# Kernel tuning notes

Hardware: AMD Instinct MI355X
Metric: run time of the kernel (lower is better)

The kernel has to match this reference:

```python
import jax, jax.numpy as jnp
import numpy as np
from jax import lax


def _sobel3d_kernels():
    # Standard separable 3D Sobel: derivative d=[-1,0,1] along one axis,
    # smoothing s=[1,2,1] along the other two. Axes order (D, H, W).
    d = np.array([-1.0, 0.0, 1.0], dtype=np.float32)
    s = np.array([1.0, 2.0, 1.0], dtype=np.float32)
    kx = np.einsum('i,j,k->ijk', d, s, s)  # derivative along D
    ky = np.einsum('i,j,k->ijk', s, d, s)  # derivative along H
    kz = np.einsum('i,j,k->ijk', s, s, d)  # derivative along W
    # Stack as [Cout=3, Cin=1, 3, 3, 3] -> one conv computes x,y,z grads at once.
    return jnp.asarray(np.stack([kx, ky, kz])[:, None])


_DN = ('NCDHW', 'OIDHW', 'NCDHW')


def _conv3(x, k):
    # x: [N, 1, D, H, W], k: [3, 1, 3, 3, 3] -> [N, 3, D-2, H-2, W-2]
    # torch F.conv3d and lax conv are both cross-correlation; VALID padding.
    return lax.conv_general_dilated(x, k, (1, 1, 1), 'VALID', dimension_numbers=_DN)


def _g2(inp, k):
    # inp: [B, D, H, W, C] (channels last, as the torch module permutes)
    b, dd, hh, ww, c = inp.shape
    x = jnp.transpose(inp, (0, 4, 1, 2, 3)).reshape(b * c, 1, dd, hh, ww)
    g1 = _conv3(x, k)                                  # [B*C, 3, D-2, H-2, W-2]
    mag = jnp.sqrt(jnp.sum(g1 * g1, axis=1, keepdims=True))  # first-order magnitude
    g2 = _conv3(mag, k)                                # [B*C, 3, D-4, H-4, W-4]
    gx, gy, gz = g2[:, 0], g2[:, 1], g2[:, 2]
    # Faithful to source: sqrt(x^2 + y^2) + z^2 (note: z is squared, not inside sqrt)
    out = jnp.sqrt(gx * gx + gy * gy) + gz * gz        # [B*C, D-4, H-4, W-4]
    return out.reshape(b, c, *out.shape[1:])


def setup_inputs() -> dict:
    key = jax.random.key(0)
    k1, k2 = jax.random.split(key)
    pred = jax.random.normal(k1, (2, 64, 64, 64, 32), dtype=jnp.float32)
    hr = jax.random.normal(k2, (2, 64, 64, 64, 32), dtype=jnp.float32)
    return {'pred': pred, 'hr': hr}


def reference(pred, hr):
    k = _sobel3d_kernels()
    return jnp.mean(jnp.abs(_g2(pred, k) - _g2(hr, k)))
```

## Files before the change

kernel.cpp:

```cpp
#include <hip/hip_runtime.h>
#include <hip/hip_fp16.h>


constexpr int BDIM = 256;
constexpr size_t IN_B = 8388608;
constexpr int IN_D = 131072;
constexpr int IN_H = 2048;
constexpr int M = 62;
constexpr int F = 60;
constexpr int C = 32;
constexpr int MROW = M * C;
constexpr size_t MAGSZ = (size_t)M * M * MROW;
constexpr size_t PLANE = (size_t)M * MROW;

__device__ __forceinline__ float2 ld2(const float* p) {
    return *reinterpret_cast<const float2*>(p);
}
__device__ __forceinline__ float2 ldh2(const __half* p) {
    return __half22float2(*reinterpret_cast<const __half2*>(p));
}

struct P1W { float2 A[4], B[4], C[4]; };

__device__ __forceinline__ void p1_plane(const float* __restrict__ col, size_t zoff,
                                         const int jr[6], P1W& W)
{
    float2 SX[6], DX[6];
#pragma unroll
    for (int j = 0; j < 6; ++j) {
        const float* p = col + zoff + jr[j];
        float2 a = ld2(p), b = ld2(p + C), c = ld2(p + 2 * C);
        SX[j] = make_float2(a.x + 2.f * b.x + c.x, a.y + 2.f * b.y + c.y);
        DX[j] = make_float2(c.x - a.x, c.y - a.y);
    }
#pragma unroll
    for (int k = 0; k < 4; ++k) {
        W.A[k] = make_float2(SX[k].x + 2.f * SX[k+1].x + SX[k+2].x,
                             SX[k].y + 2.f * SX[k+1].y + SX[k+2].y);
        W.B[k] = make_float2(SX[k+2].x - SX[k].x, SX[k+2].y - SX[k].y);
        W.C[k] = make_float2(DX[k].x + 2.f * DX[k+1].x + DX[k+2].x,
                             DX[k].y + 2.f * DX[k+1].y + DX[k+2].y);
    }
}

__device__ __forceinline__ void p1_emit(const P1W& W0, const P1W& W1, const P1W& W2,
                                        __half* __restrict__ mag, size_t cb,
                                        int z, int y0, int kmax, bool xok)
{
    if (!xok) return;
#pragma unroll
    for (int k = 0; k < 4; ++k) {
        if (k < kmax) {
            float gxx = W2.A[k].x - W0.A[k].x;
            float gxy = W2.A[k].y - W0.A[k].y;
            float gyx = W0.B[k].x + 2.f * W1.B[k].x + W2.B[k].x;
            float gyy = W0.B[k].y + 2.f * W1.B[k].y + W2.B[k].y;
            float gzx = W0.C[k].x + 2.f * W1.C[k].x + W2.C[k].x;
            float gzy = W0.C[k].y + 2.f * W1.C[k].y + W2.C[k].y;
            float mx = sqrtf(gxx * gxx + gyx * gyx + gzx * gzx);
            float my = sqrtf(gxy * gxy + gyy * gyy + gzy * gzy);
            *reinterpret_cast<__half2*>(mag + ((size_t)z * M + (y0 + k)) * MROW + cb)
                = __floats2half2_rn(mx, my);
        }
    }
}

__global__ __launch_bounds__(BDIM) void sobel_mag_stream(
    const float* __restrict__ pred, const float* __restrict__ hr,
    __half* __restrict__ magP, __half* __restrict__ magH, int b)
{
    const int xt = blockIdx.x & 3, yt = blockIdx.x >> 2;
    const int zc = blockIdx.y;
    const float* __restrict__ in  = blockIdx.z ? hr   : pred;
    __half*      __restrict__ mag = blockIdx.z ? magH : magP;

    const int y0 = yt * 4;
    const int z0 = zc * 8;
    const int zn = min(8, M - z0);
    const int kmax = min(4, M - y0);
    const int xraw = xt * 16 + (threadIdx.x >> 4);
    const bool xok = xraw < M;
    const int x = min(xraw, M - 1);
    const int c2 = (threadIdx.x & 15) << 1;

    int jr[6];
#pragma unroll
    for (int j = 0; j < 6; ++j) jr[j] = min(y0 + j, 63) * IN_H;

    const float* col = in + (size_t)b * IN_B + (size_t)x * C + c2;
    const size_t cb = (size_t)x * C + c2;

    P1W W0, W1, W2;
    p1_plane(col, (size_t)(z0 + 0) * IN_D, jr, W0);
    p1_plane(col, (size_t)(z0 + 1) * IN_D, jr, W1);
    int z = 0;
    while (true) {
        p1_plane(col, (size_t)(z0 + z + 2) * IN_D, jr, W2);
        p1_emit(W0, W1, W2, mag, cb, z0 + z, y0, kmax, xok);
        if (++z >= zn) break;
        p1_plane(col, (size_t)(z0 + z + 2) * IN_D, jr, W0);
        p1_emit(W1, W2, W0, mag, cb, z0 + z, y0, kmax, xok);
        if (++z >= zn) break;
        p1_plane(col, (size_t)(z0 + z + 2) * IN_D, jr, W1);
        p1_emit(W2, W0, W1, mag, cb, z0 + z, y0, kmax, xok);
        if (++z >= zn) break;
    }
}

struct P2W { float2 A[2], B[2], C[2]; };

__device__ __forceinline__ void p2_plane(const __half* __restrict__ col, size_t zoff, P2W& W)
{
    float2 SX[4], DX[4];
#pragma unroll
    for (int j = 0; j < 4; ++j) {
        const __half* p = col + zoff + (size_t)j * MROW;
        float2 a = ldh2(p), b = ldh2(p + C), c = ldh2(p + 2 * C);
        SX[j] = make_float2(a.x + 2.f * b.x + c.x, a.y + 2.f * b.y + c.y);
        DX[j] = make_float2(c.x - a.x, c.y - a.y);
    }
#pragma unroll
    for (int k = 0; k < 2; ++k) {
        W.A[k] = make_float2(SX[k].x + 2.f * SX[k+1].x + SX[k+2].x,
                             SX[k].y + 2.f * SX[k+1].y + SX[k+2].y);
        W.B[k] = make_float2(SX[k+2].x - SX[k].x, SX[k+2].y - SX[k].y);
        W.C[k] = make_float2(DX[k].x + 2.f * DX[k+1].x + DX[k+2].x,
                             DX[k].y + 2.f * DX[k+1].y + DX[k+2].y);
    }
}

__device__ __forceinline__ void p2_emit(const P2W& P0, const P2W& P1, const P2W& P2,
                                        const P2W& H0, const P2W& H1, const P2W& H2,
                                        float& acc)
{
#pragma unroll
    for (int k = 0; k < 2; ++k) {
        float gxPx = P2.A[k].x - P0.A[k].x;
        float gxPy = P2.A[k].y - P0.A[k].y;
        float gyPx = P0.B[k].x + 2.f * P1.B[k].x + P2.B[k].x;
        float gyPy = P0.B[k].y + 2.f * P1.B[k].y + P2.B[k].y;
        float gzPx = P0.C[k].x + 2.f * P1.C[k].x + P2.C[k].x;
        float gzPy = P0.C[k].y + 2.f * P1.C[k].y + P2.C[k].y;
        float gxHx = H2.A[k].x - H0.A[k].x;
        float gxHy = H2.A[k].y - H0.A[k].y;
        float gyHx = H0.B[k].x + 2.f * H1.B[k].x + H2.B[k].x;
        float gyHy = H0.B[k].y + 2.f * H1.B[k].y + H2.B[k].y;
        float gzHx = H0.C[k].x + 2.f * H1.C[k].x + H2.C[k].x;
        float gzHy = H0.C[k].y + 2.f * H1.C[k].y + H2.C[k].y;
        float oPx = sqrtf(gxPx * gxPx + gyPx * gyPx) + gzPx * gzPx;
        float oPy = sqrtf(gxPy * gxPy + gyPy * gyPy) + gzPy * gzPy;
        float oHx = sqrtf(gxHx * gxHx + gyHx * gyHx) + gzHx * gzHx;
        float oHy = sqrtf(gxHy * gxHy + gyHy * gyHy) + gzHy * gzHy;
        acc += fabsf(oPx - oHx) + fabsf(oPy - oHy);
    }
}

__global__ __launch_bounds__(BDIM) void sobel2_stream(
    const __half* __restrict__ magP, const __half* __restrict__ magH,
    float* __restrict__ partial, int b)
{
    const int xt = blockIdx.x & 3, yt = blockIdx.x >> 2;
    const int zc = blockIdx.y;
    const int y0 = yt * 2;
    const int z0 = zc * 10;
    const int xraw = xt * 16 + (threadIdx.x >> 4);
    const bool xok = xraw < F;
    const int x = min(xraw, F - 1);
    const int c2 = (threadIdx.x & 15) << 1;

    const size_t colo = (size_t)y0 * MROW + (size_t)x * C + c2;
    const __half* colP = magP + colo;
    const __half* colH = magH + colo;

    P2W P0, P1, P2, H0, H1, H2;
    p2_plane(colP, (size_t)(z0 + 0) * PLANE, P0);
    p2_plane(colH, (size_t)(z0 + 0) * PLANE, H0);
    p2_plane(colP, (size_t)(z0 + 1) * PLANE, P1);
    p2_plane(colH, (size_t)(z0 + 1) * PLANE, H1);
    float acc = 0.f;
    int z = 0;
    while (true) {
        p2_plane(colP, (size_t)(z0 + z + 2) * PLANE, P2);
        p2_plane(colH, (size_t)(z0 + z + 2) * PLANE, H2);
        if (xok) p2_emit(P0, P1, P2, H0, H1, H2, acc);
        if (++z >= 10) break;
        p2_plane(colP, (size_t)(z0 + z + 2) * PLANE, P0);
        p2_plane(colH, (size_t)(z0 + z + 2) * PLANE, H0);
        if (xok) p2_emit(P1, P2, P0, H1, H2, H0, acc);
        if (++z >= 10) break;
        p2_plane(colP, (size_t)(z0 + z + 2) * PLANE, P1);
        p2_plane(colH, (size_t)(z0 + z + 2) * PLANE, H1);
        if (xok) p2_emit(P2, P0, P1, H2, H0, H1, acc);
        if (++z >= 10) break;
    }

    for (int o = 32; o > 0; o >>= 1) acc += __shfl_down(acc, o, 64);
    __shared__ float sred[BDIM / 64];
    const int lane = threadIdx.x & 63, wv = threadIdx.x >> 6;
    if (lane == 0) sred[wv] = acc;
    __syncthreads();
    if (threadIdx.x == 0) {
        float t = 0.f;
#pragma unroll
        for (int i = 0; i < BDIM / 64; ++i) t += sred[i];
        partial[(size_t)b * 720 + (size_t)zc * 120 + blockIdx.x] = t;
    }
}

__global__ __launch_bounds__(BDIM) void finalize_kernel(
    const float* __restrict__ partial, float* __restrict__ out)
{
    double a = 0.0;
    for (int i = threadIdx.x; i < 1440; i += BDIM) a += (double)partial[i];
    for (int o = 32; o > 0; o >>= 1) a += __shfl_down(a, o, 64);
    __shared__ double sd[BDIM / 64];
    const int lane = threadIdx.x & 63, wv = threadIdx.x >> 6;
    if (lane == 0) sd[wv] = a;
    __syncthreads();
    if (threadIdx.x == 0) {
        double t = 0.0;
#pragma unroll
        for (int i = 0; i < BDIM / 64; ++i) t += sd[i];
        out[0] = (float)(t / 13824000.0);
    }
}

extern "C" void kernel_launch(void* const* d_in, const int* in_sizes, int n_in,
                              void* d_out, int out_size, void* d_ws, size_t ws_size,
                              hipStream_t stream)
{
    const float* pred = (const float*)d_in[0];
    const float* hr   = (const float*)d_in[1];

    float* partial = (float*)d_ws;
    __half* magP = (__half*)((char*)d_ws + 65536);
    __half* magH = magP + MAGSZ;

    for (int b = 0; b < 2; ++b) {
        sobel_mag_stream<<<dim3(64, 8, 2), BDIM, 0, stream>>>(pred, hr, magP, magH, b);
        sobel2_stream<<<dim3(120, 6), BDIM, 0, stream>>>(magP, magH, partial, b);
    }
    finalize_kernel<<<1, BDIM, 0, stream>>>(partial, (float*)d_out);
}
```

Measured before the change: 245.4 us.

## Merge batch launches and fold finalize into last-block atomic reduction

Both batch elements are now processed in a single launch of each stage by adding a batch grid dimension, with separate magnitude buffers per batch when the workspace is large enough. The separate finalize kernel is removed; the last block of the second stage, detected through an atomic counter, performs the final double-precision reduction. This cuts the launch count from five to two and lets more blocks run concurrently, but it doubles the intermediate workspace and adds an atomic per block.

```diff
diff --git a/kernel.cpp b/kernel.cpp
--- a/kernel.cpp
+++ b/kernel.cpp
@@ -12,6 +12,7 @@
 constexpr int MROW = M * C;
 constexpr size_t MAGSZ = (size_t)M * M * MROW;
 constexpr size_t PLANE = (size_t)M * MROW;
+constexpr unsigned NPART = 1440;
 
 __device__ __forceinline__ float2 ld2(const float* p) {
     return *reinterpret_cast<const float2*>(p);
@@ -67,12 +68,20 @@
 
 __global__ __launch_bounds__(BDIM) void sobel_mag_stream(
     const float* __restrict__ pred, const float* __restrict__ hr,
-    __half* __restrict__ magP, __half* __restrict__ magH, int b)
-{
+    __half* __restrict__ magP, __half* __restrict__ magH,
+    size_t magBStride, int b0, unsigned* __restrict__ counter)
+{
+    if (b0 == 0 && blockIdx.x == 0 && blockIdx.y == 0 && blockIdx.z == 0 &&
+        threadIdx.x == 0)
+        *counter = 0u;
+
     const int xt = blockIdx.x & 3, yt = blockIdx.x >> 2;
     const int zc = blockIdx.y;
-    const float* __restrict__ in  = blockIdx.z ? hr   : pred;
-    __half*      __restrict__ mag = blockIdx.z ? magH : magP;
+    const int bz = blockIdx.z;
+    const int b  = b0 + (bz >> 1);
+    const float* __restrict__ in  = (bz & 1) ? hr : pred;
+    __half*      __restrict__ mag = ((bz & 1) ? magH : magP)
+                                    + (size_t)(bz >> 1) * magBStride;
 
     const int y0 = yt * 4;
     const int z0 = zc * 8;
@@ -157,10 +166,14 @@
 
 __global__ __launch_bounds__(BDIM) void sobel2_stream(
     const __half* __restrict__ magP, const __half* __restrict__ magH,
-    float* __restrict__ partial, int b)
+    size_t magBStride, int b0,
+    float* __restrict__ partial, unsigned* __restrict__ counter,
+    float* __restrict__ out)
 {
     const int xt = blockIdx.x & 3, yt = blockIdx.x >> 2;
     const int zc = blockIdx.y;
+    const int bb = blockIdx.z;
+    const int b  = b0 + bb;
     const int y0 = yt * 2;
     const int z0 = zc * 10;
     const int xraw = xt * 16 + (threadIdx.x >> 4);
@@ -169,8 +182,8 @@
     const int c2 = (threadIdx.x & 15) << 1;
 
     const size_t colo = (size_t)y0 * MROW + (size_t)x * C + c2;
-    const __half* colP = magP + colo;
-    const __half* colH = magH + colo;
+    const __half* colP = magP + (size_t)bb * magBStride + colo;
+    const __half* colH = magH + (size_t)bb * magBStride + colo;
 
     P2W P0, P1, P2, H0, H1, H2;
     p2_plane(colP, (size_t)(z0 + 0) * PLANE, P0);
@@ -196,6 +209,7 @@
 
     for (int o = 32; o > 0; o >>= 1) acc += __shfl_down(acc, o, 64);
     __shared__ float sred[BDIM / 64];
+    __shared__ int isLast;
     const int lane = threadIdx.x & 63, wv = threadIdx.x >> 6;
     if (lane == 0) sred[wv] = acc;
     __syncthreads();
@@ -203,25 +217,30 @@
         float t = 0.f;
 #pragma unroll
         for (int i = 0; i < BDIM / 64; ++i) t += sred[i];
-        partial[(size_t)b * 720 + (size_t)zc * 120 + blockIdx.x] = t;
-    }
-}
-
-__global__ __launch_bounds__(BDIM) void finalize_kernel(
-    const float* __restrict__ partial, float* __restrict__ out)
-{
-    double a = 0.0;
-    for (int i = threadIdx.x; i < 1440; i += BDIM) a += (double)partial[i];
-    for (int o = 32; o > 0; o >>= 1) a += __shfl_down(a, o, 64);
-    __shared__ double sd[BDIM / 64];
-    const int lane = threadIdx.x & 63, wv = threadIdx.x >> 6;
-    if (lane == 0) sd[wv] = a;
+        const size_t pidx = (size_t)b * 720 + (size_t)zc * 120 + blockIdx.x;
+        __hip_atomic_store(&partial[pidx], t, __ATOMIC_RELAXED,
+                           __HIP_MEMORY_SCOPE_AGENT);
+        const unsigned old = __hip_atomic_fetch_add(counter, 1u, __ATOMIC_ACQ_REL,
+                                                    __HIP_MEMORY_SCOPE_AGENT);
+        isLast = (old == NPART - 1u) ? 1 : 0;
+    }
     __syncthreads();
-    if (threadIdx.x == 0) {
-        double t = 0.0;
-#pragma unroll
-        for (int i = 0; i < BDIM / 64; ++i) t += sd[i];
-        out[0] = (float)(t / 13824000.0);
+
+    if (isLast) {
+        double a = 0.0;
+        for (unsigned i = threadIdx.x; i < NPART; i += BDIM)
+            a += (double)__hip_atomic_load(&partial[i], __ATOMIC_RELAXED,
+                                           __HIP_MEMORY_SCOPE_AGENT);
+        for (int o = 32; o > 0; o >>= 1) a += __shfl_down(a, o, 64);
+        __shared__ double sd[BDIM / 64];
+        if (lane == 0) sd[wv] = a;
+        __syncthreads();
+        if (threadIdx.x == 0) {
+            double t = 0.0;
+#pragma unroll
+            for (int i = 0; i < BDIM / 64; ++i) t += sd[i];
+            out[0] = (float)(t / 13824000.0);
+        }
     }
 }
 
@@ -233,12 +252,26 @@
     const float* hr   = (const float*)d_in[1];
 
     float* partial = (float*)d_ws;
-    __half* magP = (__half*)((char*)d_ws + 65536);
-    __half* magH = magP + MAGSZ;
-
-    for (int b = 0; b < 2; ++b) {
-        sobel_mag_stream<<<dim3(64, 8, 2), BDIM, 0, stream>>>(pred, hr, magP, magH, b);
-        sobel2_stream<<<dim3(120, 6), BDIM, 0, stream>>>(magP, magH, partial, b);
-    }
-    finalize_kernel<<<1, BDIM, 0, stream>>>(partial, (float*)d_out);
-}
+    unsigned* counter = (unsigned*)((char*)d_ws + 32768);
+    __half* magBase = (__half*)((char*)d_ws + 65536);
+
+    const size_t needMerged = 65536 + 4 * MAGSZ * sizeof(__half);
+
+    if (ws_size >= needMerged) {
+        __half* magP = magBase;
+        __half* magH = magBase + 2 * MAGSZ;
+        sobel_mag_stream<<<dim3(64, 8, 4), BDIM, 0, stream>>>(
+            pred, hr, magP, magH, MAGSZ, 0, counter);
+        sobel2_stream<<<dim3(120, 6, 2), BDIM, 0, stream>>>(
+            magP, magH, MAGSZ, 0, partial, counter, (float*)d_out);
+    } else {
+        __half* magP = magBase;
+        __half* magH = magBase + MAGSZ;
+        for (int b = 0; b < 2; ++b) {
+            sobel_mag_stream<<<dim3(64, 8, 2), BDIM, 0, stream>>>(
+                pred, hr, magP, magH, 0, b, counter);
+            sobel2_stream<<<dim3(120, 6, 1), BDIM, 0, stream>>>(
+                magP, magH, 0, b, partial, counter, (float*)d_out);
+        }
+    }
+}
```

New measurement: 265.2 us. +8.1%, slower.

## Widen mag pass to float4 channels, shrink y-tile, fuse finalize via last-block counter

Applied to the files above, without the earlier changes.

The first Sobel pass now has each thread load float4 (four channels) instead of float2 and cover 2 output rows instead of 4. Each block covers 32 x-columns with an overlapping split (x0 = 0 or 30), so the y-halo clamp and kmax masking are gone and the grid becomes 62x8x2. The finalize kernel is removed: sobel2 blocks atomically count completions, and the last block reduces the partials and writes the mean, saving one launch. In exchange the y-halo reload ratio rises (4 input rows per 2 output rows), two x-columns per block are loaded redundantly, and correctness depends on the counter reset and atomic ordering.

```diff
diff --git a/kernel.cpp b/kernel.cpp
--- a/kernel.cpp
+++ b/kernel.cpp
@@ -12,104 +12,114 @@
 constexpr int MROW = M * C;
 constexpr size_t MAGSZ = (size_t)M * M * MROW;
 constexpr size_t PLANE = (size_t)M * MROW;
-
-__device__ __forceinline__ float2 ld2(const float* p) {
-    return *reinterpret_cast<const float2*>(p);
+constexpr unsigned NPART = 1440;
+
+__device__ __forceinline__ float4 ld4(const float* p) {
+    return *reinterpret_cast<const float4*>(p);
 }
 __device__ __forceinline__ float2 ldh2(const __half* p) {
     return __half22float2(*reinterpret_cast<const __half2*>(p));
 }
-
-struct P1W { float2 A[4], B[4], C[4]; };
+__device__ __forceinline__ float4 sm3(float4 a, float4 b, float4 c) {
+    return make_float4(a.x + 2.f * b.x + c.x, a.y + 2.f * b.y + c.y,
+                       a.z + 2.f * b.z + c.z, a.w + 2.f * b.w + c.w);
+}
+__device__ __forceinline__ float4 df2(float4 a, float4 c) {
+    return make_float4(c.x - a.x, c.y - a.y, c.z - a.z, c.w - a.w);
+}
+
+struct P1W { float4 A[2], B[2], C[2]; };
 
 __device__ __forceinline__ void p1_plane(const float* __restrict__ col, size_t zoff,
-                                         const int jr[6], P1W& W)
-{
-    float2 SX[6], DX[6];
-#pragma unroll
-    for (int j = 0; j < 6; ++j) {
-        const float* p = col + zoff + jr[j];
-        float2 a = ld2(p), b = ld2(p + C), c = ld2(p + 2 * C);
-        SX[j] = make_float2(a.x + 2.f * b.x + c.x, a.y + 2.f * b.y + c.y);
-        DX[j] = make_float2(c.x - a.x, c.y - a.y);
-    }
-#pragma unroll
-    for (int k = 0; k < 4; ++k) {
-        W.A[k] = make_float2(SX[k].x + 2.f * SX[k+1].x + SX[k+2].x,
-                             SX[k].y + 2.f * SX[k+1].y + SX[k+2].y);
-        W.B[k] = make_float2(SX[k+2].x - SX[k].x, SX[k+2].y - SX[k].y);
-        W.C[k] = make_float2(DX[k].x + 2.f * DX[k+1].x + DX[k+2].x,
-                             DX[k].y + 2.f * DX[k+1].y + DX[k+2].y);
+                                         P1W& W)
+{
+    float4 S[4], D[4];
+#pragma unroll
+    for (int r = 0; r < 4; ++r) {
+        const float* p = col + zoff + (size_t)r * IN_H;
+        float4 a = ld4(p), b = ld4(p + C), c = ld4(p + 2 * C);
+        S[r] = sm3(a, b, c);
+        D[r] = df2(a, c);
+    }
+#pragma unroll
+    for (int k = 0; k < 2; ++k) {
+        W.A[k] = sm3(S[k], S[k+1], S[k+2]);
+        W.B[k] = df2(S[k], S[k+2]);
+        W.C[k] = sm3(D[k], D[k+1], D[k+2]);
     }
 }
 
 __device__ __forceinline__ void p1_emit(const P1W& W0, const P1W& W1, const P1W& W2,
                                         __half* __restrict__ mag, size_t cb,
-                                        int z, int y0, int kmax, bool xok)
-{
-    if (!xok) return;
-#pragma unroll
-    for (int k = 0; k < 4; ++k) {
-        if (k < kmax) {
-            float gxx = W2.A[k].x - W0.A[k].x;
-            float gxy = W2.A[k].y - W0.A[k].y;
-            float gyx = W0.B[k].x + 2.f * W1.B[k].x + W2.B[k].x;
-            float gyy = W0.B[k].y + 2.f * W1.B[k].y + W2.B[k].y;
-            float gzx = W0.C[k].x + 2.f * W1.C[k].x + W2.C[k].x;
-            float gzy = W0.C[k].y + 2.f * W1.C[k].y + W2.C[k].y;
-            float mx = sqrtf(gxx * gxx + gyx * gyx + gzx * gzx);
-            float my = sqrtf(gxy * gxy + gyy * gyy + gzy * gzy);
-            *reinterpret_cast<__half2*>(mag + ((size_t)z * M + (y0 + k)) * MROW + cb)
-                = __floats2half2_rn(mx, my);
-        }
-    }
-}
-
-__global__ __launch_bounds__(BDIM) void sobel_mag_stream(
+                                        int z, int y0, bool wr)
+{
+    if (!wr) return;
+#pragma unroll
+    for (int k = 0; k < 2; ++k) {
+        float4 gx = df2(W0.A[k], W2.A[k]);
+        float4 gy = sm3(W0.B[k], W1.B[k], W2.B[k]);
+        float4 gz = sm3(W0.C[k], W1.C[k], W2.C[k]);
+        float mx = sqrtf(gx.x * gx.x + gy.x * gy.x + gz.x * gz.x);
+        float my = sqrtf(gx.y * gx.y + gy.y * gy.y + gz.y * gz.y);
+        float mz = sqrtf(gx.z * gx.z + gy.z * gy.z + gz.z * gz.z);
+        float mw = sqrtf(gx.w * gx.w + gy.w * gy.w + gz.w * gz.w);
+        union { __half2 h[2]; float2 f; } u;
+        u.h[0] = __floats2half2_rn(mx, my);
+        u.h[1] = __floats2half2_rn(mz, mw);
+        *reinterpret_cast<float2*>(mag + ((size_t)z * M + (y0 + k)) * MROW + cb)
+            = u.f;
+    }
+}
+
+__global__ __launch_bounds__(BDIM) void sobel_mag_v7(
     const float* __restrict__ pred, const float* __restrict__ hr,
-    __half* __restrict__ magP, __half* __restrict__ magH, int b)
-{
-    const int xt = blockIdx.x & 3, yt = blockIdx.x >> 2;
+    __half* __restrict__ magP, __half* __restrict__ magH,
+    int b, unsigned* __restrict__ counter, int zeroCtr)
+{
+    if (zeroCtr && blockIdx.x == 0 && blockIdx.y == 0 && blockIdx.z == 0 &&
+        threadIdx.x == 0)
+        __hip_atomic_store(counter, 0u, __ATOMIC_RELAXED,
+                           __HIP_MEMORY_SCOPE_AGENT);
+
+    const int xt = blockIdx.x & 1, yt = blockIdx.x >> 1;
     const int zc = blockIdx.y;
     const float* __restrict__ in  = blockIdx.z ? hr   : pred;
     __half*      __restrict__ mag = blockIdx.z ? magH : magP;
 
-    const int y0 = yt * 4;
+    const int c4 = (threadIdx.x & 7) << 2;
+    const int xl = threadIdx.x >> 3;
+    const int x0 = xt * 30;
+    const int x  = x0 + xl;
+    const bool wr = (xt == 0) || (xl >= 2);
+    const int y0 = yt * 2;
     const int z0 = zc * 8;
     const int zn = min(8, M - z0);
-    const int kmax = min(4, M - y0);
-    const int xraw = xt * 16 + (threadIdx.x >> 4);
-    const bool xok = xraw < M;
-    const int x = min(xraw, M - 1);
-    const int c2 = (threadIdx.x & 15) << 1;
-
-    int jr[6];
-#pragma unroll
-    for (int j = 0; j < 6; ++j) jr[j] = min(y0 + j, 63) * IN_H;
-
-    const float* col = in + (size_t)b * IN_B + (size_t)x * C + c2;
-    const size_t cb = (size_t)x * C + c2;
+
+    const float* col = in + (size_t)b * IN_B + (size_t)y0 * IN_H
+                          + (size_t)x * C + c4;
+    const size_t cb = (size_t)x * C + c4;
 
     P1W W0, W1, W2;
-    p1_plane(col, (size_t)(z0 + 0) * IN_D, jr, W0);
-    p1_plane(col, (size_t)(z0 + 1) * IN_D, jr, W1);
+    p1_plane(col, (size_t)(z0 + 0) * IN_D, W0);
+    p1_plane(col, (size_t)(z0 + 1) * IN_D, W1);
     int z = 0;
     while (true) {
-        p1_plane(col, (size_t)(z0 + z + 2) * IN_D, jr, W2);
-        p1_emit(W0, W1, W2, mag, cb, z0 + z, y0, kmax, xok);
+        p1_plane(col, (size_t)(z0 + z + 2) * IN_D, W2);
+        p1_emit(W0, W1, W2, mag, cb, z0 + z, y0, wr);
         if (++z >= zn) break;
-        p1_plane(col, (size_t)(z0 + z + 2) * IN_D, jr, W0);
-        p1_emit(W1, W2, W0, mag, cb, z0 + z, y0, kmax, xok);
+        p1_plane(col, (size_t)(z0 + z + 2) * IN_D, W0);
+        p1_emit(W1, W2, W0, mag, cb, z0 + z, y0, wr);
         if (++z >= zn) break;
-        p1_plane(col, (size_t)(z0 + z + 2) * IN_D, jr, W1);
-        p1_emit(W2, W0, W1, mag, cb, z0 + z, y0, kmax, xok);
+        p1_plane(col, (size_t)(z0 + z + 2) * IN_D, W1);
+        p1_emit(W2, W0, W1, mag, cb, z0 + z, y0, wr);
         if (++z >= zn) break;
     }
 }
 
 struct P2W { float2 A[2], B[2], C[2]; };
 
-__device__ __forceinline__ void p2_plane(const __half* __restrict__ col, size_t zoff, P2W& W)
+__device__ __forceinline__ void p2_plane(const __half* __restrict__ col, size_t zoff,
+                                         P2W& W)
 {
     float2 SX[4], DX[4];
 #pragma unroll
@@ -155,9 +165,10 @@
     }
 }
 
-__global__ __launch_bounds__(BDIM) void sobel2_stream(
+__global__ __launch_bounds__(BDIM) void sobel2_v7(
     const __half* __restrict__ magP, const __half* __restrict__ magH,
-    float* __restrict__ partial, int b)
+    int b, float* __restrict__ partial, unsigned* __restrict__ counter,
+    float* __restrict__ out)
 {
     const int xt = blockIdx.x & 3, yt = blockIdx.x >> 2;
     const int zc = blockIdx.y;
@@ -196,6 +207,7 @@
 
     for (int o = 32; o > 0; o >>= 1) acc += __shfl_down(acc, o, 64);
     __shared__ float sred[BDIM / 64];
+    __shared__ int isLast;
     const int lane = threadIdx.x & 63, wv = threadIdx.x >> 6;
     if (lane == 0) sred[wv] = acc;
     __syncthreads();
@@ -203,25 +215,30 @@
         float t = 0.f;
 #pragma unroll
         for (int i = 0; i < BDIM / 64; ++i) t += sred[i];
-        partial[(size_t)b * 720 + (size_t)zc * 120 + blockIdx.x] = t;
-    }
-}
-
-__global__ __launch_bounds__(BDIM) void finalize_kernel(
-    const float* __restrict__ partial, float* __restrict__ out)
-{
-    double a = 0.0;
-    for (int i = threadIdx.x; i < 1440; i += BDIM) a += (double)partial[i];
-    for (int o = 32; o > 0; o >>= 1) a += __shfl_down(a, o, 64);
-    __shared__ double sd[BDIM / 64];
-    const int lane = threadIdx.x & 63, wv = threadIdx.x >> 6;
-    if (lane == 0) sd[wv] = a;
+        const size_t pidx = (size_t)b * 720 + (size_t)zc * 120 + blockIdx.x;
+        __hip_atomic_store(&partial[pidx], t, __ATOMIC_RELAXED,
+                           __HIP_MEMORY_SCOPE_AGENT);
+        const unsigned old = __hip_atomic_fetch_add(counter, 1u, __ATOMIC_ACQ_REL,
+                                                    __HIP_MEMORY_SCOPE_AGENT);
+        isLast = (old == NPART - 1u) ? 1 : 0;
+    }
     __syncthreads();
-    if (threadIdx.x == 0) {
-        double t = 0.0;
-#pragma unroll
-        for (int i = 0; i < BDIM / 64; ++i) t += sd[i];
-        out[0] = (float)(t / 13824000.0);
+
+    if (isLast) {
+        double a = 0.0;
+        for (unsigned i = threadIdx.x; i < NPART; i += BDIM)
+            a += (double)__hip_atomic_load(&partial[i], __ATOMIC_RELAXED,
+                                           __HIP_MEMORY_SCOPE_AGENT);
+        for (int o = 32; o > 0; o >>= 1) a += __shfl_down(a, o, 64);
+        __shared__ double sd[BDIM / 64];
+        if (lane == 0) sd[wv] = a;
+        __syncthreads();
+        if (threadIdx.x == 0) {
+            double t = 0.0;
+#pragma unroll
+            for (int i = 0; i < BDIM / 64; ++i) t += sd[i];
+            out[0] = (float)(t / 13824000.0);
+        }
     }
 }
 
@@ -233,12 +250,14 @@
     const float* hr   = (const float*)d_in[1];
 
     float* partial = (float*)d_ws;
+    unsigned* counter = (unsigned*)((char*)d_ws + 32768);
     __half* magP = (__half*)((char*)d_ws + 65536);
     __half* magH = magP + MAGSZ;
 
     for (int b = 0; b < 2; ++b) {
-        sobel_mag_stream<<<dim3(64, 8, 2), BDIM, 0, stream>>>(pred, hr, magP, magH, b);
-        sobel2_stream<<<dim3(120, 6), BDIM, 0, stream>>>(magP, magH, partial, b);
-    }
-    finalize_kernel<<<1, BDIM, 0, stream>>>(partial, (float*)d_out);
-}
+        sobel_mag_v7<<<dim3(62, 8, 2), BDIM, 0, stream>>>(
+            pred, hr, magP, magH, b, counter, b == 0 ? 1 : 0);
+        sobel2_v7<<<dim3(120, 6), BDIM, 0, stream>>>(
+            magP, magH, b, partial, counter, (float*)d_out);
+    }
+}
```

Result: slower. 257.5 us (+5.0%).
